# Kernel tuning notes

Measured on AMD Instinct MI355X. Metric: run time of the kernel, lower is better.

Reference implementation:

```python
import jax, jax.numpy as jnp
import numpy as np

E, D, H = 8, 2048, 2048  # num_experts, features, expert_dim
B, L, K = 2, 2048, 2


def setup_inputs() -> dict:
    key = jax.random.key(0)
    k1, k2, k3, k4, k5, k6 = jax.random.split(key, 6)
    x = jax.random.normal(k1, (B, L, D), dtype=jnp.float32)
    w = jax.random.uniform(k2, (B, L, K), dtype=jnp.float32)
    weights = w / jnp.sum(w, axis=-1, keepdims=True)  # normalised routing weights
    expert_indices = jax.random.randint(k3, (B, L, K), 0, E, dtype=jnp.int64)
    gate_up = jax.random.normal(k4, (E, D, 2 * H), dtype=jnp.float32) * 0.02
    down = jax.random.normal(k5, (E, H, D), dtype=jnp.float32) * 0.02
    per_expert_scale = 1.0 + 0.01 * jax.random.normal(k6, (E,), dtype=jnp.float32)
    return {"x": x, "weights": weights, "expert_indices": expert_indices,
            "gate_up": gate_up, "down": down, "per_expert_scale": per_expert_scale}


def reference(x, weights, expert_indices, gate_up, down, per_expert_scale):
    Bb, Ll, Dd = x.shape
    Ee = gate_up.shape[0]
    N = Bb * Ll
    xf = x.reshape(N, Dd)                                   # [N, D]
    idx = expert_indices.reshape(N, -1)                     # [N, K]
    wts = weights.reshape(N, -1)                            # [N, K]
    # combine[n, e] = sum_k weights[n,k] * 1[idx[n,k]==e]; scale folded in.
    onehot = jax.nn.one_hot(idx, Ee, dtype=x.dtype)         # [N, K, E]
    combine = jnp.einsum('nk,nke->ne', wts, onehot) * per_expert_scale  # [N, E]
    # Dense per-expert GatedMLP (grouped GEMM across all experts).
    h = jnp.einsum('nd,edh->enh', xf, gate_up)              # [E, N, 2H]
    gate, up = jnp.split(h, 2, axis=-1)
    act = jax.nn.gelu(gate, approximate=False) * up         # exact gelu, as torch F.gelu
    y = jnp.einsum('enh,ehd->end', act, down)               # [E, N, D]
    out = jnp.einsum('end,ne->nd', y, combine)              # weighted combine over experts
    return out.reshape(Bb, Ll, Dd)
```

## Files before the change

kernel.cpp:

```cpp
#include <hip/hip_runtime.h>
#include <math.h>

#define EXPERTS 8
#define DDIM 2048
#define HDIM 2048
#define NTOK 4096
#define NPAIR 8192
#define MAXSLOT 9216
#define MAXTILE 72

typedef _Float16 f16;
typedef __attribute__((ext_vector_type(8))) _Float16 f16x8;
typedef __attribute__((ext_vector_type(4))) _Float16 f16x4;
typedef __attribute__((ext_vector_type(4))) float f32x4;

#define XF_OFF   0ull
#define ACT_OFF  16777216ull
#define Y_OFF    54525952ull
#define CTRL_OFF 92274688ull
#define CTRL_INTS 26792

#define BARRIER() asm volatile("s_barrier" ::: "memory")
#define VMCNT(n)  asm volatile("s_waitcnt vmcnt(" #n ")" ::: "memory")
#define LGKM0()   asm volatile("s_waitcnt lgkmcnt(0)" ::: "memory")

__device__ __forceinline__ void gload_lds16(const void* g, void* l) {
  __builtin_amdgcn_global_load_lds(
      (const __attribute__((address_space(1))) unsigned int*)g,
      (__attribute__((address_space(3))) unsigned int*)l,
      16, 0, 0);
}

__device__ __forceinline__ int swz(int r) { return (r >> 1) & 3; }

__global__ void k_detect(const int* __restrict__ w, int* flag) {
  int i = blockIdx.x * blockDim.x + threadIdx.x;
  if (i < NPAIR / 2 && w[2 * i + 1] != 0) atomicOr(flag, 1);
}

__device__ __forceinline__ int expert_of(const int* idx, int is32, int p) {
  return is32 ? idx[p] : idx[2 * p];
}

__global__ void k_count(const int* __restrict__ idx, const int* __restrict__ flag,
                        int* cnt) {
  int p = blockIdx.x * blockDim.x + threadIdx.x;
  if (p < NPAIR) atomicAdd(&cnt[expert_of(idx, *flag, p)], 1);
}

__global__ void k_plan(const int* __restrict__ cnt, int* cursor,
                       int* tile_e, int* tile_r0, int* n_tiles) {
  if (blockIdx.x == 0 && threadIdx.x == 0) {
    int off = 0, nt = 0;
    for (int e = 0; e < EXPERTS; ++e) {
      cursor[e] = off;
      int t = (cnt[e] + 127) >> 7;
      for (int i = 0; i < t; ++i) { tile_e[nt] = e; tile_r0[nt] = off + i * 128; ++nt; }
      off += t * 128;
    }
    *n_tiles = nt;
  }
}

__global__ void k_assign(const int* __restrict__ idx, const int* __restrict__ flag,
                         const float* __restrict__ wts, const float* __restrict__ scale,
                         int* cursor, int* slot_tok, int* tok_slot, float* slot_w) {
  int p = blockIdx.x * blockDim.x + threadIdx.x;
  if (p < NPAIR) {
    int e = expert_of(idx, *flag, p);
    int pos = atomicAdd(&cursor[e], 1);
    slot_tok[pos] = p >> 1;
    tok_slot[p] = pos;
    slot_w[pos] = wts[p] * scale[e];
  }
}

__global__ void k_cvt_x(const float* __restrict__ in, f16* __restrict__ out) {
  int i = blockIdx.x * blockDim.x + threadIdx.x;
  float4 v = ((const float4*)in)[i];
  f16x4 o = {(f16)v.x, (f16)v.y, (f16)v.z, (f16)v.w};
  ((f16x4*)out)[i] = o;
}

template <int G1>
__global__ __launch_bounds__(256, 3) void k_gemm(
    const f16* __restrict__ Asrc, const float* __restrict__ W,
    const int* __restrict__ slot_tok,
    const int* __restrict__ tile_e, const int* __restrict__ tile_r0,
    const int* __restrict__ n_tiles, f16* __restrict__ dst) {
  __shared__ __align__(16) f16 smem[2][8192];

  const int bx = blockIdx.y;
  if (bx >= *n_tiles) return;
  const int nt = blockIdx.x;
  const int e = tile_e[bx];
  const int m0 = tile_r0[bx];
  const int LDB = G1 ? 4096 : 2048;

  const int tid = threadIdx.x;
  const int lane = tid & 63;
  const int wv = tid >> 6;
  const int wm = wv >> 1;
  const int wn = wv & 1;
  const int fr = lane & 15;
  const int fhi = lane >> 4;

  const f16* aS[2];
#pragma unroll
  for (int i = 0; i < 2; ++i) {
    const int r = i * 64 + (tid >> 2);
    size_t arow = G1 ? (size_t)slot_tok[m0 + r] : (size_t)(m0 + r);
    aS[i] = Asrc + arow * 2048 + ((tid & 3) ^ swz(r)) * 8;
  }
  auto gloadA = [&](int s, int kt) {
#pragma unroll
    for (int i = 0; i < 2; ++i)
      gload_lds16(aS[i] + (size_t)kt * 32, &smem[s][i * 2048 + tid * 8]);
  };

  const int cp = tid & 63;
  const int kf = tid >> 6;
  int gcol;
  if (G1) gcol = (cp < 32) ? nt * 64 + 2 * cp : 2048 + nt * 64 + (2 * cp - 64);
  else    gcol = nt * 128 + 2 * cp;
  const float* bP = W + (size_t)e * 2048 * LDB + (size_t)(8 * kf) * LDB + gcol;
  const int bbase = 2 * cp * 32 + ((kf ^ (cp & 3)) << 3);

  float2 qe[8], qo[8];
  auto loadB = [&](float2 (&q)[8], int kt) {
    const float* p = bP + (size_t)kt * 32 * LDB;
#pragma unroll
    for (int j = 0; j < 8; ++j) q[j] = *(const float2*)(p + j * LDB);
  };
  auto writeB = [&](float2 (&q)[8], int s) {
    f16x8 wa = {(f16)q[0].x, (f16)q[1].x, (f16)q[2].x, (f16)q[3].x,
                (f16)q[4].x, (f16)q[5].x, (f16)q[6].x, (f16)q[7].x};
    f16x8 wb = {(f16)q[0].y, (f16)q[1].y, (f16)q[2].y, (f16)q[3].y,
                (f16)q[4].y, (f16)q[5].y, (f16)q[6].y, (f16)q[7].y};
    f16* B = &smem[s][4096];
    *(f16x8*)&B[bbase] = wa;
    *(f16x8*)&B[bbase + 32] = wb;
  };

  int ctv[4];
#pragma unroll
  for (int ci = 0; ci < 4; ++ci) {
    if (G1) ctv[ci] = (ci < 2) ? (wn * 2 + ci) : (4 + wn * 2 + (ci - 2));
    else    ctv[ci] = wn * 4 + ci;
  }

  f32x4 acc[4][4];
#pragma unroll
  for (int i = 0; i < 4; ++i)
#pragma unroll
    for (int j = 0; j < 4; ++j) acc[i][j] = (f32x4){0.f, 0.f, 0.f, 0.f};

  auto compute = [&](int s) {
    const f16* As = &smem[s][0];
    const f16* Bs = &smem[s][4096];
    f16x8 af[4], bf[4];
#pragma unroll
    for (int mi = 0; mi < 4; ++mi) {
      const int r = wm * 64 + mi * 16 + fr;
      af[mi] = *(const f16x8*)&As[r * 32 + ((fhi ^ swz(r)) << 3)];
    }
#pragma unroll
    for (int ci = 0; ci < 4; ++ci) {
      const int c = ctv[ci] * 16 + fr;
      bf[ci] = *(const f16x8*)&Bs[c * 32 + ((fhi ^ swz(c)) << 3)];
    }
    __builtin_amdgcn_s_setprio(1);
#pragma unroll
    for (int mi = 0; mi < 4; ++mi)
#pragma unroll
      for (int ci = 0; ci < 4; ++ci)
        acc[mi][ci] = __builtin_amdgcn_mfma_f32_16x16x32_f16(af[mi], bf[ci],
                                                             acc[mi][ci], 0, 0, 0);
    __builtin_amdgcn_s_setprio(0);
  };

  const int NT = 64;

  loadB(qe, 0);
  loadB(qo, 1);
  gloadA(0, 0);
  VMCNT(10);
  writeB(qe, 0);
  __builtin_amdgcn_sched_barrier(0);
  loadB(qe, 2);
  VMCNT(8);
  LGKM0();
  BARRIER();

  auto giter = [&](int kt, float2 (&Q)[8]) {
    const int s = kt & 1;
    if (kt + 1 < NT) {
      gloadA(s ^ 1, kt + 1);
      writeB(Q, s ^ 1);
    }
    __builtin_amdgcn_sched_barrier(0);
    if (kt + 3 < NT) loadB(Q, kt + 3);
    compute(s);
    if (kt + 1 < NT) {
      if (kt + 3 < NT) { VMCNT(8); } else { VMCNT(0); }
      LGKM0();
      BARRIER();
    }
  };

  for (int kt = 0; kt < NT; kt += 2) {
    giter(kt, qo);
    giter(kt + 1, qe);
  }

  if (G1) {
#pragma unroll
    for (int mi = 0; mi < 4; ++mi)
#pragma unroll
      for (int ci = 0; ci < 2; ++ci)
#pragma unroll
        for (int rg = 0; rg < 4; ++rg) {
          const int row = m0 + wm * 64 + mi * 16 + fhi * 4 + rg;
          const int col = nt * 64 + (wn * 2 + ci) * 16 + fr;
          const float g = acc[mi][ci][rg];
          const float u = acc[mi][ci + 2][rg];
          const float a = 0.5f * g * (1.0f + erff(g * 0.70710678118654752f)) * u;
          dst[(size_t)row * 2048 + col] = (f16)a;
        }
  } else {
#pragma unroll
    for (int mi = 0; mi < 4; ++mi)
#pragma unroll
      for (int ci = 0; ci < 4; ++ci)
#pragma unroll
        for (int rg = 0; rg < 4; ++rg) {
          const int row = m0 + wm * 64 + mi * 16 + fhi * 4 + rg;
          const int col = nt * 128 + wn * 64 + ci * 16 + fr;
          dst[(size_t)row * 2048 + col] = (f16)acc[mi][ci][rg];
        }
  }
}

__global__ void k_combine(const f16* __restrict__ y, const float* __restrict__ slot_w,
                          const int* __restrict__ tok_slot, float* __restrict__ out) {
  const int gid = blockIdx.x * blockDim.x + threadIdx.x;
  const int tok = gid >> 8;
  const int c = (gid & 255) * 8;
  const int s0 = tok_slot[2 * tok], s1 = tok_slot[2 * tok + 1];
  const float w0 = slot_w[s0], w1 = slot_w[s1];
  const f16x8 v0 = *(const f16x8*)&y[(size_t)s0 * 2048 + c];
  const f16x8 v1 = *(const f16x8*)&y[(size_t)s1 * 2048 + c];
  float o[8];
#pragma unroll
  for (int j = 0; j < 8; ++j) o[j] = w0 * (float)v0[j] + w1 * (float)v1[j];
  float4* op = (float4*)&out[(size_t)tok * 2048 + c];
  op[0] = (float4){o[0], o[1], o[2], o[3]};
  op[1] = (float4){o[4], o[5], o[6], o[7]};
}

extern "C" void kernel_launch(void* const* d_in, const int* in_sizes, int n_in,
                              void* d_out, int out_size, void* d_ws, size_t ws_size,
                              hipStream_t stream) {
  const float* x = (const float*)d_in[0];
  const float* wts = (const float*)d_in[1];
  const int* idx = (const int*)d_in[2];
  const float* gup = (const float*)d_in[3];
  const float* dwn = (const float*)d_in[4];
  const float* scale = (const float*)d_in[5];
  float* out = (float*)d_out;

  char* ws = (char*)d_ws;
  f16* xf = (f16*)(ws + XF_OFF);
  f16* act = (f16*)(ws + ACT_OFF);
  f16* y = (f16*)(ws + Y_OFF);
  int* ctrl = (int*)(ws + CTRL_OFF);
  int* slot_tok = ctrl;
  int* tok_slot = ctrl + 9216;
  int* cnt = ctrl + 17408;
  int* cursor = ctrl + 17416;
  int* tile_e = ctrl + 17424;
  int* tile_r0 = ctrl + 17496;
  int* n_tiles = ctrl + 17568;
  int* is32 = ctrl + 17569;
  float* slot_w = (float*)(ctrl + 17576);

  hipMemsetAsync(ctrl, 0, (size_t)CTRL_INTS * sizeof(int), stream);

  k_detect<<<NPAIR / 2 / 256, 256, 0, stream>>>(idx, is32);
  k_count<<<NPAIR / 256, 256, 0, stream>>>(idx, is32, cnt);
  k_plan<<<1, 1, 0, stream>>>(cnt, cursor, tile_e, tile_r0, n_tiles);
  k_assign<<<NPAIR / 256, 256, 0, stream>>>(idx, is32, wts, scale, cursor,
                                            slot_tok, tok_slot, slot_w);
  k_cvt_x<<<NTOK * DDIM / 4 / 256, 256, 0, stream>>>(x, xf);
  k_gemm<1><<<dim3(32, MAXTILE), 256, 0, stream>>>(xf, gup, slot_tok, tile_e,
                                                   tile_r0, n_tiles, act);
  k_gemm<0><<<dim3(16, MAXTILE), 256, 0, stream>>>(act, dwn, slot_tok, tile_e,
                                                   tile_r0, n_tiles, y);
  k_combine<<<NTOK, 256, 0, stream>>>(y, slot_w, tok_slot, out);
}
```

Measured before the change: 524.8 us.

## Widen grouped GEMM to 512 threads with K=64 tiles and single-buffered B prefetch

The grouped GEMM kernels now run 8 waves per block instead of 4, each wave computing a 64x32 sub-tile, and the K step per stage doubles from 32 to 64, which halves the number of barrier-synchronised iterations. LDS per stage doubles and the swizzle becomes an 8-way XOR to fit the wider rows. The B prefetch drops from two register buffers running three steps ahead to a single buffer one step ahead, so each wave holds fewer registers, at the cost of less latency hiding for the fp32 weight loads. Occupancy moves from 3 blocks of 256 threads to 2 blocks of 512.

```diff
diff --git a/kernel.cpp b/kernel.cpp
--- a/kernel.cpp
+++ b/kernel.cpp
@@ -30,8 +30,6 @@
       (__attribute__((address_space(3))) unsigned int*)l,
       16, 0, 0);
 }
-
-__device__ __forceinline__ int swz(int r) { return (r >> 1) & 3; }
 
 __global__ void k_detect(const int* __restrict__ w, int* flag) {
   int i = blockIdx.x * blockDim.x + threadIdx.x;
@@ -83,12 +81,12 @@
 }
 
 template <int G1>
-__global__ __launch_bounds__(256, 3) void k_gemm(
+__global__ __launch_bounds__(512, 2) void k_gemm(
     const f16* __restrict__ Asrc, const float* __restrict__ W,
     const int* __restrict__ slot_tok,
     const int* __restrict__ tile_e, const int* __restrict__ tile_r0,
     const int* __restrict__ n_tiles, f16* __restrict__ dst) {
-  __shared__ __align__(16) f16 smem[2][8192];
+  __shared__ __align__(16) f16 smem[2][16384];
 
   const int bx = blockIdx.y;
   if (bx >= *n_tiles) return;
@@ -100,22 +98,22 @@
   const int tid = threadIdx.x;
   const int lane = tid & 63;
   const int wv = tid >> 6;
-  const int wm = wv >> 1;
-  const int wn = wv & 1;
+  const int wrM = wv >> 2;
+  const int wcl = wv & 3;
   const int fr = lane & 15;
   const int fhi = lane >> 4;
 
   const f16* aS[2];
 #pragma unroll
   for (int i = 0; i < 2; ++i) {
-    const int r = i * 64 + (tid >> 2);
+    const int r = i * 64 + (tid >> 3);
     size_t arow = G1 ? (size_t)slot_tok[m0 + r] : (size_t)(m0 + r);
-    aS[i] = Asrc + arow * 2048 + ((tid & 3) ^ swz(r)) * 8;
+    aS[i] = Asrc + arow * 2048 + ((tid & 7) ^ (r & 7)) * 8;
   }
   auto gloadA = [&](int s, int kt) {
 #pragma unroll
     for (int i = 0; i < 2; ++i)
-      gload_lds16(aS[i] + (size_t)kt * 32, &smem[s][i * 2048 + tid * 8]);
+      gload_lds16(aS[i] + (size_t)kt * 64, &smem[s][i * 4096 + tid * 8]);
   };
 
   const int cp = tid & 63;
@@ -124,118 +122,115 @@
   if (G1) gcol = (cp < 32) ? nt * 64 + 2 * cp : 2048 + nt * 64 + (2 * cp - 64);
   else    gcol = nt * 128 + 2 * cp;
   const float* bP = W + (size_t)e * 2048 * LDB + (size_t)(8 * kf) * LDB + gcol;
-  const int bbase = 2 * cp * 32 + ((kf ^ (cp & 3)) << 3);
-
-  float2 qe[8], qo[8];
-  auto loadB = [&](float2 (&q)[8], int kt) {
-    const float* p = bP + (size_t)kt * 32 * LDB;
+  const int bbase = 8192 + 2 * cp * 64 + ((kf ^ (cp & 7)) << 3);
+
+  float2 q[8];
+  auto loadB = [&](int kt) {
+    const float* p = bP + (size_t)kt * 64 * LDB;
 #pragma unroll
     for (int j = 0; j < 8; ++j) q[j] = *(const float2*)(p + j * LDB);
   };
-  auto writeB = [&](float2 (&q)[8], int s) {
+  auto writeB = [&](int s) {
     f16x8 wa = {(f16)q[0].x, (f16)q[1].x, (f16)q[2].x, (f16)q[3].x,
                 (f16)q[4].x, (f16)q[5].x, (f16)q[6].x, (f16)q[7].x};
     f16x8 wb = {(f16)q[0].y, (f16)q[1].y, (f16)q[2].y, (f16)q[3].y,
                 (f16)q[4].y, (f16)q[5].y, (f16)q[6].y, (f16)q[7].y};
-    f16* B = &smem[s][4096];
-    *(f16x8*)&B[bbase] = wa;
-    *(f16x8*)&B[bbase + 32] = wb;
-  };
-
-  int ctv[4];
-#pragma unroll
-  for (int ci = 0; ci < 4; ++ci) {
-    if (G1) ctv[ci] = (ci < 2) ? (wn * 2 + ci) : (4 + wn * 2 + (ci - 2));
-    else    ctv[ci] = wn * 4 + ci;
-  }
-
-  f32x4 acc[4][4];
+    *(f16x8*)&smem[s][bbase] = wa;
+    *(f16x8*)&smem[s][bbase + 64] = wb;
+  };
+
+  int ctv[2];
+#pragma unroll
+  for (int ci = 0; ci < 2; ++ci)
+    ctv[ci] = G1 ? (wcl + ci * 4) : (wcl * 2 + ci);
+
+  f32x4 acc[4][2];
 #pragma unroll
   for (int i = 0; i < 4; ++i)
 #pragma unroll
-    for (int j = 0; j < 4; ++j) acc[i][j] = (f32x4){0.f, 0.f, 0.f, 0.f};
+    for (int j = 0; j < 2; ++j) acc[i][j] = (f32x4){0.f, 0.f, 0.f, 0.f};
 
   auto compute = [&](int s) {
     const f16* As = &smem[s][0];
-    const f16* Bs = &smem[s][4096];
-    f16x8 af[4], bf[4];
-#pragma unroll
-    for (int mi = 0; mi < 4; ++mi) {
-      const int r = wm * 64 + mi * 16 + fr;
-      af[mi] = *(const f16x8*)&As[r * 32 + ((fhi ^ swz(r)) << 3)];
-    }
-#pragma unroll
-    for (int ci = 0; ci < 4; ++ci) {
-      const int c = ctv[ci] * 16 + fr;
-      bf[ci] = *(const f16x8*)&Bs[c * 32 + ((fhi ^ swz(c)) << 3)];
-    }
+    const f16* Bs = &smem[s][0];
+    f16x8 af[4][2], bf[2][2];
+#pragma unroll
+    for (int mi = 0; mi < 4; ++mi)
+#pragma unroll
+      for (int k0 = 0; k0 < 2; ++k0) {
+        const int r = wrM * 64 + mi * 16 + fr;
+        af[mi][k0] = *(const f16x8*)&As[r * 64 + (((k0 * 4 + fhi) ^ (r & 7)) << 3)];
+      }
+#pragma unroll
+    for (int ci = 0; ci < 2; ++ci)
+#pragma unroll
+      for (int k0 = 0; k0 < 2; ++k0) {
+        const int c = ctv[ci] * 16 + fr;
+        bf[ci][k0] = *(const f16x8*)&Bs[8192 + c * 64 +
+                                        (((k0 * 4 + fhi) ^ ((c >> 1) & 7)) << 3)];
+      }
     __builtin_amdgcn_s_setprio(1);
 #pragma unroll
-    for (int mi = 0; mi < 4; ++mi)
-#pragma unroll
-      for (int ci = 0; ci < 4; ++ci)
-        acc[mi][ci] = __builtin_amdgcn_mfma_f32_16x16x32_f16(af[mi], bf[ci],
-                                                             acc[mi][ci], 0, 0, 0);
+    for (int k0 = 0; k0 < 2; ++k0)
+#pragma unroll
+      for (int mi = 0; mi < 4; ++mi)
+#pragma unroll
+        for (int ci = 0; ci < 2; ++ci)
+          acc[mi][ci] = __builtin_amdgcn_mfma_f32_16x16x32_f16(
+              af[mi][k0], bf[ci][k0], acc[mi][ci], 0, 0, 0);
     __builtin_amdgcn_s_setprio(0);
   };
 
-  const int NT = 64;
-
-  loadB(qe, 0);
-  loadB(qo, 1);
+  const int NT = 32;
+
+  loadB(0);
   gloadA(0, 0);
-  VMCNT(10);
-  writeB(qe, 0);
+  VMCNT(2);
+  writeB(0);
   __builtin_amdgcn_sched_barrier(0);
-  loadB(qe, 2);
+  loadB(1);
   VMCNT(8);
   LGKM0();
   BARRIER();
 
-  auto giter = [&](int kt, float2 (&Q)[8]) {
+  for (int kt = 0; kt < NT; ++kt) {
     const int s = kt & 1;
     if (kt + 1 < NT) {
       gloadA(s ^ 1, kt + 1);
-      writeB(Q, s ^ 1);
+      VMCNT(2);
+      writeB(s ^ 1);
+      __builtin_amdgcn_sched_barrier(0);
+      if (kt + 2 < NT) loadB(kt + 2);
     }
-    __builtin_amdgcn_sched_barrier(0);
-    if (kt + 3 < NT) loadB(Q, kt + 3);
     compute(s);
     if (kt + 1 < NT) {
-      if (kt + 3 < NT) { VMCNT(8); } else { VMCNT(0); }
+      if (kt + 2 < NT) { VMCNT(8); } else { VMCNT(0); }
       LGKM0();
       BARRIER();
     }
-  };
-
-  for (int kt = 0; kt < NT; kt += 2) {
-    giter(kt, qo);
-    giter(kt + 1, qe);
   }
 
   if (G1) {
 #pragma unroll
     for (int mi = 0; mi < 4; ++mi)
 #pragma unroll
+      for (int rg = 0; rg < 4; ++rg) {
+        const int row = m0 + wrM * 64 + mi * 16 + fhi * 4 + rg;
+        const int col = nt * 64 + wcl * 16 + fr;
+        const float g = acc[mi][0][rg];
+        const float u = acc[mi][1][rg];
+        const float a = 0.5f * g * (1.0f + erff(g * 0.70710678118654752f)) * u;
+        dst[(size_t)row * 2048 + col] = (f16)a;
+      }
+  } else {
+#pragma unroll
+    for (int mi = 0; mi < 4; ++mi)
+#pragma unroll
       for (int ci = 0; ci < 2; ++ci)
 #pragma unroll
         for (int rg = 0; rg < 4; ++rg) {
-          const int row = m0 + wm * 64 + mi * 16 + fhi * 4 + rg;
-          const int col = nt * 64 + (wn * 2 + ci) * 16 + fr;
-          const float g = acc[mi][ci][rg];
-          const float u = acc[mi][ci + 2][rg];
-          const float a = 0.5f * g * (1.0f + erff(g * 0.70710678118654752f)) * u;
-          dst[(size_t)row * 2048 + col] = (f16)a;
-        }
-  } else {
-#pragma unroll
-    for (int mi = 0; mi < 4; ++mi)
-#pragma unroll
-      for (int ci = 0; ci < 4; ++ci)
-#pragma unroll
-        for (int rg = 0; rg < 4; ++rg) {
-          const int row = m0 + wm * 64 + mi * 16 + fhi * 4 + rg;
-          const int col = nt * 128 + wn * 64 + ci * 16 + fr;
+          const int row = m0 + wrM * 64 + mi * 16 + fhi * 4 + rg;
+          const int col = nt * 128 + (wcl * 2 + ci) * 16 + fr;
           dst[(size_t)row * 2048 + col] = (f16)acc[mi][ci][rg];
         }
   }
@@ -292,9 +287,9 @@
   k_assign<<<NPAIR / 256, 256, 0, stream>>>(idx, is32, wts, scale, cursor,
                                             slot_tok, tok_slot, slot_w);
   k_cvt_x<<<NTOK * DDIM / 4 / 256, 256, 0, stream>>>(x, xf);
-  k_gemm<1><<<dim3(32, MAXTILE), 256, 0, stream>>>(xf, gup, slot_tok, tile_e,
+  k_gemm<1><<<dim3(32, MAXTILE), 512, 0, stream>>>(xf, gup, slot_tok, tile_e,
                                                    tile_r0, n_tiles, act);
-  k_gemm<0><<<dim3(16, MAXTILE), 256, 0, stream>>>(act, dwn, slot_tok, tile_e,
+  k_gemm<0><<<dim3(16, MAXTILE), 512, 0, stream>>>(act, dwn, slot_tok, tile_e,
                                                    tile_r0, n_tiles, y);
   k_combine<<<NTOK, 256, 0, stream>>>(y, slot_w, tok_slot, out);
 }
```

Result: faster. 487.5 us (-7.1%).
